# Kernel tuning notes

Measured on AMD Instinct MI355X. Metric: run time of the kernel, lower is better.

The kernel has to match this reference:

```python
import jax, jax.numpy as jnp
import numpy as np

N = 1048576            # num nodes == num edges (required by the original's indexing)
C = 64                 # in_channels
FIRST = N // 3         # analogue of the hardcoded 8-of-24 fixed-weight prefix


def setup_inputs() -> dict:
    key = jax.random.key(0)
    k1, k2, k3 = jax.random.split(key, 3)
    x = jax.random.normal(k1, (N, C), dtype=jnp.float32)
    edge_index = jax.random.randint(k2, (2, N), 0, N, dtype=jnp.int64)
    # EdgeWeightLayer.lin : Linear(in_channels -> out_channels*heads = 1)
    lin_w = jax.random.normal(k3, (1, C), dtype=jnp.float32) / np.float32(np.sqrt(C))
    lin_b = jnp.zeros((1,), dtype=jnp.float32)
    w1 = jnp.array([1.0], dtype=jnp.float32)    # fixed_edge_weights_1
    w2 = jnp.array([-0.5], dtype=jnp.float32)   # learnable_edge_weights_2
    w3 = jnp.array([1.5], dtype=jnp.float32)    # learnable_edge_weights_3
    return {"x": x, "lin_w": lin_w, "lin_b": lin_b, "w1": w1, "w2": w2, "w3": w3,
            "edge_index": edge_index}


def reference(x, lin_w, lin_b, w1, w2, w3, edge_index):
    n = x.shape[0]
    # --- EdgeWeightLayer: add self loops, message = lin(x_j - x_i), aggr='add' at target i
    loop = jnp.arange(n, dtype=edge_index.dtype)
    src = jnp.concatenate([edge_index[0], loop])   # j
    dst = jnp.concatenate([edge_index[1], loop])   # i
    msg = (x[src] - x[dst]) @ lin_w.T + lin_b      # [2N, 1]
    learned = jax.ops.segment_sum(msg, dst, num_segments=n)  # [n, 1] per-node scores

    # --- final_edge_scores construction (generalized 24 -> N, 8 -> FIRST)
    idx = jnp.arange(n)
    base = jnp.where(idx < FIRST, w1[0],
                     jnp.where((idx - FIRST) % 2 == 0, w2[0], w3[0]))
    scores = base[:, None] + jnp.where(idx >= FIRST, learned[:, 0], 0.0)[:, None]  # [n,1]

    # --- per-edge gather -> scalar scale -> scatter-add (the explicit loop in torch)
    e = edge_index.shape[1]
    agg = jax.ops.segment_sum(x[edge_index[0]] * scores[:e],
                              edge_index[1], num_segments=n)   # [n, C]
    return jax.nn.relu(agg)
```

## Files before the change

kernel.cpp:

```cpp
#include <hip/hip_runtime.h>

#define C 64

typedef float fx4 __attribute__((ext_vector_type(4)));

__global__ void dot_kernel(const float4* __restrict__ x4,
                           const float4* __restrict__ w4,
                           const float* __restrict__ lin_b,
                           float* __restrict__ d,
                           float* __restrict__ learned, int n) {
    int gtid = blockIdx.x * blockDim.x + threadIdx.x;
    int wave = gtid >> 6;
    int lane = threadIdx.x & 63;
    int sub  = lane >> 4;
    int sl   = lane & 15;
    int node = wave * 4 + sub;
    if (node >= n) return;
    float4 v = x4[(size_t)node * 16 + sl];
    float4 w = w4[sl];
    float t = v.x * w.x + v.y * w.y + v.z * w.z + v.w * w.w;
    t += __shfl_xor(t, 8, 64);
    t += __shfl_xor(t, 4, 64);
    t += __shfl_xor(t, 2, 64);
    t += __shfl_xor(t, 1, 64);
    if (sl == 0) {
        d[node] = t;
        learned[node] = lin_b[0];
    }
}

__global__ void hist_kernel(const int* __restrict__ ei,
                            const float* __restrict__ d,
                            const float* __restrict__ lin_b,
                            float* __restrict__ learned,
                            int* __restrict__ count,
                            int* __restrict__ rank,
                            int n, int first) {
    int e = blockIdx.x * blockDim.x + threadIdx.x;
    if (e >= n) return;
    int t = ei[n + e];
    rank[e] = atomicAdd(&count[t], 1);
    if (t >= first) {
        int s = ei[e];
        atomicAdd(&learned[t], d[s] - d[t] + lin_b[0]);
    }
}

__global__ void scan1_kernel(const int* __restrict__ count,
                             int* __restrict__ off,
                             int* __restrict__ partial) {
    __shared__ int sh[256];
    int tid = threadIdx.x;
    int gid = blockIdx.x * 256 + tid;
    int v = count[gid];
    sh[tid] = v;
    __syncthreads();
    for (int o = 1; o < 256; o <<= 1) {
        int t = (tid >= o) ? sh[tid - o] : 0;
        __syncthreads();
        sh[tid] += t;
        __syncthreads();
    }
    off[gid] = sh[tid] - v;
    if (tid == 255) partial[blockIdx.x] = sh[255];
}

__global__ void scan2_kernel(int* __restrict__ partial, int nb) {
    __shared__ int sh[256];
    int tid = threadIdx.x;
    int chunk = nb / 256;
    int base = tid * chunk;
    int sum = 0;
    for (int k = 0; k < chunk; ++k) sum += partial[base + k];
    sh[tid] = sum;
    __syncthreads();
    for (int o = 1; o < 256; o <<= 1) {
        int t = (tid >= o) ? sh[tid - o] : 0;
        __syncthreads();
        sh[tid] += t;
        __syncthreads();
    }
    int running = sh[tid] - sum;
    for (int k = 0; k < chunk; ++k) {
        int v = partial[base + k];
        partial[base + k] = running;
        running += v;
    }
}

__global__ void reorder_kernel(const int* __restrict__ ei,
                               const float* __restrict__ learned,
                               const int* __restrict__ off,
                               const int* __restrict__ partial,
                               const int* __restrict__ rank,
                               int2* __restrict__ srcscore,
                               const float* __restrict__ w1,
                               const float* __restrict__ w2,
                               const float* __restrict__ w3,
                               int n, int first) {
    int e = blockIdx.x * blockDim.x + threadIdx.x;
    if (e >= n) return;
    float score;
    if (e < first) {
        score = w1[0];
    } else {
        float base = (((e - first) & 1) == 0) ? w2[0] : w3[0];
        score = base + learned[e];
    }
    int s = ei[e];
    int t = ei[n + e];
    int pos = off[t] + partial[t >> 8] + rank[e];
    srcscore[pos] = make_int2(s, __float_as_int(score));
}

__global__ void gather_kernel(const float4* __restrict__ x4,
                              const int* __restrict__ off,
                              const int* __restrict__ partial,
                              const int2* __restrict__ srcscore,
                              float4* __restrict__ out4, int n) {
    int gtid = blockIdx.x * blockDim.x + threadIdx.x;
    int wave = gtid >> 6;
    int lane = threadIdx.x & 63;
    int sub  = lane >> 4;
    int sl   = lane & 15;
    int node = wave * 4 + sub;
    if (node >= n) return;
    int beg = off[node] + partial[node >> 8];
    int end = (node + 1 < n) ? (off[node + 1] + partial[(node + 1) >> 8]) : n;
    float4 acc = make_float4(0.f, 0.f, 0.f, 0.f);
    int base = sub << 4;
    for (int j0 = beg; j0 < end; j0 += 16) {
        int rem = end - j0;
        int m = (rem < 16) ? rem : 16;
        int2 p = make_int2(0, 0);
        if (sl < m) p = srcscore[j0 + sl];
        for (int k = 0; k < m; ++k) {
            int   src = __shfl(p.x, base + k, 64);
            float s   = __int_as_float(__shfl(p.y, base + k, 64));
            float4 v = x4[(size_t)src * 16 + sl];
            acc.x += v.x * s;
            acc.y += v.y * s;
            acc.z += v.z * s;
            acc.w += v.w * s;
        }
    }
    acc.x = fmaxf(acc.x, 0.f);
    acc.y = fmaxf(acc.y, 0.f);
    acc.z = fmaxf(acc.z, 0.f);
    acc.w = fmaxf(acc.w, 0.f);
    fx4 av;
    av.x = acc.x; av.y = acc.y; av.z = acc.z; av.w = acc.w;
    __builtin_nontemporal_store(av, (fx4*)&out4[(size_t)node * 16 + sl]);
}

extern "C" void kernel_launch(void* const* d_in, const int* in_sizes, int n_in,
                              void* d_out, int out_size, void* d_ws, size_t ws_size,
                              hipStream_t stream) {
    const float* x     = (const float*)d_in[0];
    const float* lin_w = (const float*)d_in[1];
    const float* lin_b = (const float*)d_in[2];
    const float* w1    = (const float*)d_in[3];
    const float* w2    = (const float*)d_in[4];
    const float* w3    = (const float*)d_in[5];
    const int*   ei    = (const int*)d_in[6];
    float* out = (float*)d_out;

    const int n = in_sizes[0] / C;
    const int first = n / 3;
    const int nb = n / 256;

    float* d_dot    = (float*)d_ws;
    float* learned  = d_dot + n;
    int*   count    = (int*)(learned + n);
    int*   off      = count + n;
    int*   rank     = off + n;
    int2*  srcscore = (int2*)(rank + n);
    int*   partial  = (int*)(srcscore + n);

    hipMemsetAsync(count, 0, (size_t)n * sizeof(int), stream);

    dot_kernel<<<dim3(n / 16), dim3(256), 0, stream>>>(
        (const float4*)x, (const float4*)lin_w, lin_b, d_dot, learned, n);
    hist_kernel<<<dim3(nb), dim3(256), 0, stream>>>(ei, d_dot, lin_b, learned,
                                                    count, rank, n, first);
    scan1_kernel<<<dim3(nb), dim3(256), 0, stream>>>(count, off, partial);
    scan2_kernel<<<dim3(1), dim3(256), 0, stream>>>(partial, nb);
    reorder_kernel<<<dim3(nb), dim3(256), 0, stream>>>(ei, learned, off, partial,
                                                       rank, srcscore, w1, w2, w3,
                                                       n, first);
    gather_kernel<<<dim3(n / 16), dim3(256), 0, stream>>>(
        (const float4*)x, off, partial, srcscore, (float4*)out, n);
}
```

Before: 638.7 us.

## Fuse histogram into dot kernel and learned-score scatter into scan pass

The degree histogram and rank atomics move into the dot-product kernel, and the learned-score atomic accumulation moves into the first scan kernel. One launch is removed, and the learned array is zeroed by a widened memset instead of being initialised to the bias. The bias is added once in the reorder step. This lets the histogram atomics overlap with the dot-product loads. The cost is that the scatter now runs inside the scan kernel ahead of its barriers, and ei is re-read there.

```diff
diff --git a/kernel.cpp b/kernel.cpp
--- a/kernel.cpp
+++ b/kernel.cpp
@@ -4,12 +4,20 @@
 
 typedef float fx4 __attribute__((ext_vector_type(4)));
 
-__global__ void dot_kernel(const float4* __restrict__ x4,
-                           const float4* __restrict__ w4,
-                           const float* __restrict__ lin_b,
-                           float* __restrict__ d,
-                           float* __restrict__ learned, int n) {
+__global__ void dot_hist_kernel(const float4* __restrict__ x4,
+                                const float4* __restrict__ w4,
+                                const int* __restrict__ ei,
+                                float* __restrict__ d,
+                                int* __restrict__ count,
+                                int* __restrict__ rank,
+                                int n) {
     int gtid = blockIdx.x * blockDim.x + threadIdx.x;
+
+    if (gtid < n) {
+        int t = ei[n + gtid];
+        rank[gtid] = atomicAdd(&count[t], 1);
+    }
+
     int wave = gtid >> 6;
     int lane = threadIdx.x & 63;
     int sub  = lane >> 4;
@@ -23,42 +31,34 @@
     t += __shfl_xor(t, 4, 64);
     t += __shfl_xor(t, 2, 64);
     t += __shfl_xor(t, 1, 64);
-    if (sl == 0) {
-        d[node] = t;
-        learned[node] = lin_b[0];
-    }
+    if (sl == 0) d[node] = t;
 }
 
-__global__ void hist_kernel(const int* __restrict__ ei,
-                            const float* __restrict__ d,
-                            const float* __restrict__ lin_b,
-                            float* __restrict__ learned,
-                            int* __restrict__ count,
-                            int* __restrict__ rank,
-                            int n, int first) {
-    int e = blockIdx.x * blockDim.x + threadIdx.x;
-    if (e >= n) return;
-    int t = ei[n + e];
-    rank[e] = atomicAdd(&count[t], 1);
-    if (t >= first) {
-        int s = ei[e];
-        atomicAdd(&learned[t], d[s] - d[t] + lin_b[0]);
-    }
-}
-
-__global__ void scan1_kernel(const int* __restrict__ count,
-                             int* __restrict__ off,
-                             int* __restrict__ partial) {
+__global__ void scatter_scan1_kernel(const int* __restrict__ ei,
+                                     const float* __restrict__ d,
+                                     const float* __restrict__ lin_b,
+                                     float* __restrict__ learned,
+                                     const int* __restrict__ count,
+                                     int* __restrict__ off,
+                                     int* __restrict__ partial,
+                                     int n, int first) {
     __shared__ int sh[256];
     int tid = threadIdx.x;
     int gid = blockIdx.x * 256 + tid;
+
+    int t = ei[n + gid];
+    if (t >= first) {
+        int s = ei[gid];
+        atomicAdd(&learned[t], d[s] - d[t] + lin_b[0]);
+    }
+
     int v = count[gid];
     sh[tid] = v;
     __syncthreads();
     for (int o = 1; o < 256; o <<= 1) {
-        int t = (tid >= o) ? sh[tid - o] : 0;
+        int tt = (tid >= o) ? sh[tid - o] : 0;
         __syncthreads();
-        sh[tid] += t;
+        sh[tid] += tt;
         __syncthreads();
     }
     off[gid] = sh[tid] - v;
@@ -94,6 +94,7 @@
                                const int* __restrict__ partial,
                                const int* __restrict__ rank,
                                int2* __restrict__ srcscore,
+                               const float* __restrict__ lin_b,
                                const float* __restrict__ w1,
                                const float* __restrict__ w2,
                                const float* __restrict__ w3,
@@ -105,7 +106,7 @@
         score = w1[0];
     } else {
         float base = (((e - first) & 1) == 0) ? w2[0] : w3[0];
-        score = base + learned[e];
+        score = base + lin_b[0] + learned[e];
     }
     int s = ei[e];
     int t = ei[n + e];
@@ -177,17 +178,16 @@
     int2*  srcscore = (int2*)(rank + n);
     int*   partial  = (int*)(srcscore + n);
 
-    hipMemsetAsync(count, 0, (size_t)n * sizeof(int), stream);
+    hipMemsetAsync(learned, 0, (size_t)2 * n * sizeof(int), stream);
 
-    dot_kernel<<<dim3(n / 16), dim3(256), 0, stream>>>(
-        (const float4*)x, (const float4*)lin_w, lin_b, d_dot, learned, n);
-    hist_kernel<<<dim3(nb), dim3(256), 0, stream>>>(ei, d_dot, lin_b, learned,
-                                                    count, rank, n, first);
-    scan1_kernel<<<dim3(nb), dim3(256), 0, stream>>>(count, off, partial);
+    dot_hist_kernel<<<dim3(n / 16), dim3(256), 0, stream>>>(
+        (const float4*)x, (const float4*)lin_w, ei, d_dot, count, rank, n);
+    scatter_scan1_kernel<<<dim3(nb), dim3(256), 0, stream>>>(
+        ei, d_dot, lin_b, learned, count, off, partial, n, first);
     scan2_kernel<<<dim3(1), dim3(256), 0, stream>>>(partial, nb);
     reorder_kernel<<<dim3(nb), dim3(256), 0, stream>>>(ei, learned, off, partial,
-                                                       rank, srcscore, w1, w2, w3,
-                                                       n, first);
+                                                       rank, srcscore, lin_b,
+                                                       w1, w2, w3, n, first);
     gather_kernel<<<dim3(n / 16), dim3(256), 0, stream>>>(
         (const float4*)x, off, partial, srcscore, (float4*)out, n);
 }
```

After: 635.2 us. About the same (-0.5%).
